# Kernel optimization log

Measured on AMD Instinct MI355X. Metric: run time of the kernel, lower is better.

Reference implementation:

```python
import jax, jax.numpy as jnp
import numpy as np


def _sage_conv(h_src, h_dst, src, dst, W_neigh, W_self, b, n_dst):
    # mean aggregation over in-neighbors of each dst node
    msg = h_src[src]                                             # [E, F]
    s = jax.ops.segment_sum(msg, dst, num_segments=n_dst)        # [n_dst, F]
    deg = jax.ops.segment_sum(jnp.ones_like(dst, dtype=h_src.dtype), dst,
                              num_segments=n_dst)                # [n_dst]
    h_neigh = s / jnp.maximum(deg, 1.0)[:, None]
    # DGL SAGEConv (mean): fc_self(h_dst) + fc_neigh(h_neigh) + bias
    return h_dst @ W_self + h_neigh @ W_neigh + b


def setup_inputs() -> dict:
    key = jax.random.key(0)
    ks = jax.random.split(key, 10)
    N1, N2, N3 = 200000, 40000, 8000
    E1, E2 = 1280000, 256000
    IN, H, C = 128, 256, 47
    return {
        "x": jax.random.normal(ks[0], (N1, IN), dtype=jnp.float32),
        "src1": jax.random.randint(ks[1], (E1,), 0, N1, dtype=jnp.int32),
        "dst1": jax.random.randint(ks[2], (E1,), 0, N2, dtype=jnp.int32),
        "src2": jax.random.randint(ks[3], (E2,), 0, N2, dtype=jnp.int32),
        "dst2": jax.random.randint(ks[4], (E2,), 0, N3, dtype=jnp.int32),
        "n_dst1": N2,
        "n_dst2": N3,
        "W_self1": jax.random.normal(ks[5], (IN, H), dtype=jnp.float32) * (1.0 / np.sqrt(IN)),
        "W_neigh1": jax.random.normal(ks[6], (IN, H), dtype=jnp.float32) * (1.0 / np.sqrt(IN)),
        "b1": jnp.zeros((H,), dtype=jnp.float32),
        "W_self2": jax.random.normal(ks[7], (H, C), dtype=jnp.float32) * (1.0 / np.sqrt(H)),
        "W_neigh2": jax.random.normal(ks[8], (H, C), dtype=jnp.float32) * (1.0 / np.sqrt(H)),
        "b2": jnp.zeros((C,), dtype=jnp.float32),
    }


def reference(x, src1, dst1, src2, dst2, n_dst1, n_dst2,
              W_self1, W_neigh1, b1, W_self2, W_neigh2, b2):
    h_dst = x[:n_dst1]                                            # [N2, IN]
    h = _sage_conv(x, h_dst, src1, dst1, W_neigh1, W_self1, b1, n_dst1)
    h = jax.nn.relu(h)                                            # [N2, H]
    h_dst2 = h[:n_dst2]                                           # [N3, H]
    out = _sage_conv(h, h_dst2, src2, dst2, W_neigh2, W_self2, b2, n_dst2)
    return out                                                    # [N3, C]
```

## Files before the change

### kernel.cpp

```cpp
#include <hip/hip_runtime.h>
#include <hip/hip_bf16.h>
#include <cstddef>


#define N1_SRC 200000
#define N2_DST 40000
#define N2_PAD 40064
#define N3_DST 8000
#define IN_F 128
#define H_F 256
#define C_F 47

#define BSHIFT 7
#define SRCB 18
#define NB1 313
#define NB2 63
#define CAST_BLOCKS 6250

typedef short bf16x8 __attribute__((ext_vector_type(8)));
typedef float f32x4 __attribute__((ext_vector_type(4)));

__device__ __forceinline__ float bf2f(ushort u) {
    union { uint i; float f; } v; v.i = ((uint)u) << 16; return v.f;
}
__device__ __forceinline__ ushort f2bf(float f) {
    union { float f; uint i; } v; v.f = f;
    uint r = v.i + 0x7FFF + ((v.i >> 16) & 1);
    return (ushort)(r >> 16);
}
__device__ __forceinline__ uint pack2(float lo, float hi) {
    return (uint)f2bf(lo) | ((uint)f2bf(hi) << 16);
}
__device__ __forceinline__ void acc8(float* a, uint4 v) {
    a[0] += bf2f((ushort)(v.x & 0xffff)); a[1] += bf2f((ushort)(v.x >> 16));
    a[2] += bf2f((ushort)(v.y & 0xffff)); a[3] += bf2f((ushort)(v.y >> 16));
    a[4] += bf2f((ushort)(v.z & 0xffff)); a[5] += bf2f((ushort)(v.z >> 16));
    a[6] += bf2f((ushort)(v.w & 0xffff)); a[7] += bf2f((ushort)(v.w >> 16));
}


__global__ __launch_bounds__(256) void prep_kernel(
    const float* __restrict__ x, ushort* __restrict__ xb,
    const int* __restrict__ dst1, int* __restrict__ bcnt1, int E1,
    const int* __restrict__ dst2, int* __restrict__ bcnt2, int E2,
    const float* __restrict__ Wself1, const float* __restrict__ Wneigh1,
    ushort* __restrict__ WT1,
    const float* __restrict__ Wself2, const float* __restrict__ Wneigh2,
    ushort* __restrict__ WT2,
    const float* __restrict__ b2, float* __restrict__ bias2p) {
    __shared__ int cnt[NB1];
    int bx = blockIdx.x, t = threadIdx.x;
    if (bx < CAST_BLOCKS) {
        const float4* in4 = (const float4*)x;
        ushort4* out4 = (ushort4*)xb;
        int base = bx * 1024 + t;
#pragma unroll
        for (int j = 0; j < 4; ++j) {
            float4 v = in4[base + j * 256];
            ushort4 o;
            o.x = f2bf(v.x); o.y = f2bf(v.y); o.z = f2bf(v.z); o.w = f2bf(v.w);
            out4[base + j * 256] = o;
        }
        return;
    }
    bx -= CAST_BLOCKS;
    if (bx < NB1 + NB2) {
        const int* dst = (bx < NB1) ? dst1 : dst2;
        int* bcnt = (bx < NB1) ? bcnt1 : bcnt2;
        int E = (bx < NB1) ? E1 : E2;
        int hb = (bx < NB1) ? bx : bx - NB1;
        for (int i = t; i < NB1; i += 256) cnt[i] = 0;
        __syncthreads();
        int base = hb * 4096 + t;
#pragma unroll
        for (int i = 0; i < 16; ++i) {
            int e = base + i * 256;
            if (e < E) atomicAdd(&cnt[dst[e] >> BSHIFT], 1);
        }
        __syncthreads();
        for (int i = t; i < NB1; i += 256) {
            int c = cnt[i];
            if (c) atomicAdd(&bcnt[i], c);
        }
        return;
    }
    bx -= NB1 + NB2;
    if (bx < H_F) {
        int n = bx;
        for (int k = t; k < 2 * IN_F; k += 256) {
            float v = (k < IN_F) ? Wself1[(size_t)k * H_F + n]
                                 : Wneigh1[(size_t)(k - IN_F) * H_F + n];
            WT1[(size_t)n * (2 * IN_F) + k] = f2bf(v);
        }
        return;
    }
    bx -= H_F;
    if (bx < 64) {
        int n = bx;
        for (int k = t; k < 2 * H_F; k += 256) {
            float v = 0.f;
            if (n < C_F) v = (k < H_F) ? Wself2[(size_t)k * C_F + n]
                                       : Wneigh2[(size_t)(k - H_F) * C_F + n];
            WT2[(size_t)n * (2 * H_F) + k] = f2bf(v);
        }
        return;
    }
    bx -= 64;
    if (bx == 0 && t < 64) bias2p[t] = (t < C_F) ? b2[t] : 0.f;
}


__global__ void bucket_scan2(
    const int* __restrict__ bcnt1, int* __restrict__ boff1, int* __restrict__ gcur1,
    int E1, int* __restrict__ off1,
    const int* __restrict__ bcnt2, int* __restrict__ boff2, int* __restrict__ gcur2,
    int E2, int* __restrict__ off2) {
    __shared__ int smem[512];
    int t = threadIdx.x;
    int L = blockIdx.x;
    const int nb = L ? NB2 : NB1;
    const int* bcnt = L ? bcnt2 : bcnt1;
    int* boff = L ? boff2 : boff1;
    int* gcur = L ? gcur2 : gcur1;
    int E = L ? E2 : E1;
    int* offs = L ? off2 : off1;
    int nd = L ? N3_DST : N2_DST;
    int v = (t < nb) ? bcnt[t] : 0;
    smem[t] = v;
    __syncthreads();
    for (int off = 1; off < 512; off <<= 1) {
        int tv = (t >= off) ? smem[t - off] : 0;
        __syncthreads();
        smem[t] += tv;
        __syncthreads();
    }
    if (t < nb) { int e = smem[t] - v; boff[t] = e; gcur[t] = e; }
    if (t == 0) { boff[nb] = E; offs[nd] = E; }
}


__global__ __launch_bounds__(256) void bin_pass1m(
    const int* __restrict__ src1, const int* __restrict__ dst1,
    int* __restrict__ gcur1, uint* __restrict__ temp1, int E1,
    const int* __restrict__ src2, const int* __restrict__ dst2,
    int* __restrict__ gcur2, uint* __restrict__ temp2, int E2) {
    __shared__ int cnt[NB1];
    __shared__ int rnk[NB1];
    __shared__ int gbase[NB1];
    int L = blockIdx.y;
    const int* src = L ? src2 : src1;
    const int* dst = L ? dst2 : dst1;
    int* gcur = L ? gcur2 : gcur1;
    uint* temp = L ? temp2 : temp1;
    int E = L ? E2 : E1;
    int t = threadIdx.x;
    int e0 = blockIdx.x * 4096;
    if (e0 >= E) return;
    for (int i = t; i < NB1; i += 256) { cnt[i] = 0; rnk[i] = 0; }
    __syncthreads();
#pragma unroll
    for (int i = 0; i < 16; ++i) {
        int e = e0 + i * 256 + t;
        if (e < E) atomicAdd(&cnt[dst[e] >> BSHIFT], 1);
    }
    __syncthreads();
    for (int b = t; b < NB1; b += 256) {
        int c = cnt[b];
        gbase[b] = c ? atomicAdd(&gcur[b], c) : 0;
    }
    __syncthreads();
#pragma unroll
    for (int i = 0; i < 16; ++i) {
        int e = e0 + i * 256 + t;
        if (e < E) {
            int d = dst[e];
            int b = d >> BSHIFT;
            int r = atomicAdd(&rnk[b], 1);
            uint val = ((uint)(d & 127) << SRCB) | (uint)src[e];
            temp[gbase[b] + r] = val;
        }
    }
}


__global__ __launch_bounds__(256) void bin_pass2m(
    const uint* __restrict__ temp1, const int* __restrict__ boff1,
    int* __restrict__ off1, int* __restrict__ edges1,
    const uint* __restrict__ temp2, const int* __restrict__ boff2,
    int* __restrict__ off2, int* __restrict__ edges2) {
    constexpr int DPB = 128;
    __shared__ int cnt[DPB];
    __shared__ int scn[DPB];
    __shared__ int obase[DPB];
    __shared__ int rnk[DPB];
    int b = blockIdx.x, t = threadIdx.x;
    int L = (b >= NB1);
    int lb = L ? b - NB1 : b;
    const uint* temp = L ? temp2 : temp1;
    const int* boff = L ? boff2 : boff1;
    int* offsets = L ? off2 : off1;
    int* edges = L ? edges2 : edges1;
    int nd = L ? N3_DST : N2_DST;
    int dbase = lb << BSHIFT;
    if (t < DPB) { cnt[t] = 0; rnk[t] = 0; }
    __syncthreads();
    int beg = boff[lb], end = boff[lb + 1];
    for (int i = beg + t; i < end; i += 256) {
        atomicAdd(&cnt[temp[i] >> SRCB], 1);
    }
    __syncthreads();
    int v = (t < DPB) ? cnt[t] : 0;
    if (t < DPB) scn[t] = v;
    __syncthreads();
    for (int off = 1; off < DPB; off <<= 1) {
        int tv = (t >= off && t < DPB) ? scn[t - off] : 0;
        __syncthreads();
        if (t < DPB) scn[t] += tv;
        __syncthreads();
    }
    if (t < DPB) {
        int ob = beg + scn[t] - v;
        obase[t] = ob;
        if (dbase + t < nd) offsets[dbase + t] = ob;
    }
    __syncthreads();
    for (int i = beg + t; i < end; i += 256) {
        uint val = temp[i];
        int dlow = (int)(val >> SRCB);
        int s = (int)(val & ((1u << SRCB) - 1));
        int r = atomicAdd(&rnk[dlow], 1);
        edges[obase[dlow] + r] = s;
    }
}


__global__ __launch_bounds__(256) void gather_mean_f128(
    const ushort* __restrict__ xb, const int* __restrict__ edges,
    const int* __restrict__ offsets, ushort* __restrict__ outb) {
    int d = (blockIdx.x << 2) | (threadIdx.x >> 6);
    int lane = threadIdx.x & 63;
    int eslot = lane >> 4, lpos = lane & 15;
    int beg = offsets[d], end = offsets[d + 1];
    float a[8] = {};
    int i = beg;
    for (; i + 16 <= end; i += 16) {
        int e0 = edges[i + eslot];
        int e1 = edges[i + 4 + eslot];
        int e2 = edges[i + 8 + eslot];
        int e3 = edges[i + 12 + eslot];
        uint4 v0 = ((const uint4*)(xb + (size_t)e0 * IN_F))[lpos];
        uint4 v1 = ((const uint4*)(xb + (size_t)e1 * IN_F))[lpos];
        uint4 v2 = ((const uint4*)(xb + (size_t)e2 * IN_F))[lpos];
        uint4 v3 = ((const uint4*)(xb + (size_t)e3 * IN_F))[lpos];
        acc8(a, v0); acc8(a, v1); acc8(a, v2); acc8(a, v3);
    }
    for (; i < end; i += 4) {
        if (i + eslot < end) {
            int e = edges[i + eslot];
            uint4 v = ((const uint4*)(xb + (size_t)e * IN_F))[lpos];
            acc8(a, v);
        }
    }
#pragma unroll
    for (int j = 0; j < 8; ++j) {
        a[j] += __shfl_xor(a[j], 16);
        a[j] += __shfl_xor(a[j], 32);
    }
    if (eslot == 0) {
        float inv = 1.0f / fmaxf((float)(end - beg), 1.0f);
        uint4 o;
        o.x = pack2(a[0] * inv, a[1] * inv);
        o.y = pack2(a[2] * inv, a[3] * inv);
        o.z = pack2(a[4] * inv, a[5] * inv);
        o.w = pack2(a[6] * inv, a[7] * inv);
        ((uint4*)(outb + (size_t)d * IN_F))[lpos] = o;
    }
}

__global__ __launch_bounds__(256) void gather_mean_f256(
    const ushort* __restrict__ hb, const int* __restrict__ edges,
    const int* __restrict__ offsets, ushort* __restrict__ outb) {
    int d = (blockIdx.x << 2) | (threadIdx.x >> 6);
    int lane = threadIdx.x & 63;
    int eslot = lane >> 5, lpos = lane & 31;
    int beg = offsets[d], end = offsets[d + 1];
    float a[8] = {};
    int i = beg;
    for (; i + 8 <= end; i += 8) {
        int e0 = edges[i + eslot];
        int e1 = edges[i + 2 + eslot];
        int e2 = edges[i + 4 + eslot];
        int e3 = edges[i + 6 + eslot];
        uint4 v0 = ((const uint4*)(hb + (size_t)e0 * H_F))[lpos];
        uint4 v1 = ((const uint4*)(hb + (size_t)e1 * H_F))[lpos];
        uint4 v2 = ((const uint4*)(hb + (size_t)e2 * H_F))[lpos];
        uint4 v3 = ((const uint4*)(hb + (size_t)e3 * H_F))[lpos];
        acc8(a, v0); acc8(a, v1); acc8(a, v2); acc8(a, v3);
    }
    for (; i < end; i += 2) {
        if (i + eslot < end) {
            int e = edges[i + eslot];
            uint4 v = ((const uint4*)(hb + (size_t)e * H_F))[lpos];
            acc8(a, v);
        }
    }
#pragma unroll
    for (int j = 0; j < 8; ++j) {
        a[j] += __shfl_xor(a[j], 32);
    }
    if (eslot == 0) {
        float inv = 1.0f / fmaxf((float)(end - beg), 1.0f);
        uint4 o;
        o.x = pack2(a[0] * inv, a[1] * inv);
        o.y = pack2(a[2] * inv, a[3] * inv);
        o.z = pack2(a[4] * inv, a[5] * inv);
        o.w = pack2(a[6] * inv, a[7] * inv);
        ((uint4*)(outb + (size_t)d * H_F))[lpos] = o;
    }
}


__global__ __launch_bounds__(256) void sage_mfma_gemm128(
    const ushort* __restrict__ Aself, const ushort* __restrict__ Aneigh,
    const ushort* __restrict__ WT, const float* __restrict__ bias,
    ushort* __restrict__ Cout) {
    constexpr int LDL = 72;
    __shared__ __align__(16) ushort A_lds[128 * LDL];
    __shared__ __align__(16) ushort B_lds[128 * LDL];
    int t = threadIdx.x;
    int bn = blockIdx.x * 128, bm = blockIdx.y * 128;
    int lane = t & 63, w = t >> 6;
    int wr = w >> 1, wc = w & 1;
    int ln = lane & 15, kh = lane >> 4;
    f32x4 acc[4][4] = {};
    for (int kt0 = 0; kt0 < 256; kt0 += 64) {
#pragma unroll
        for (int c = 0; c < 4; ++c) {
            int id = c * 256 + t;
            int row = id >> 3;
            int kc = (id & 7) * 8;
            int k = kt0 + kc;
            const ushort* sa = (k < IN_F)
                                   ? Aself + (size_t)(bm + row) * IN_F + k
                                   : Aneigh + (size_t)(bm + row) * IN_F + (k - IN_F);
            *(float4*)&A_lds[row * LDL + kc] = *(const float4*)sa;
            *(float4*)&B_lds[row * LDL + kc] =
                *(const float4*)(WT + (size_t)(bn + row) * 256 + k);
        }
        __syncthreads();
#pragma unroll
        for (int kt = 0; kt < 2; ++kt) {
            bf16x8 aF[4], bF[4];
#pragma unroll
            for (int m = 0; m < 4; ++m)
                aF[m] = *(const bf16x8*)&A_lds[(wr * 64 + m * 16 + ln) * LDL + kt * 32 + kh * 8];
#pragma unroll
            for (int n = 0; n < 4; ++n)
                bF[n] = *(const bf16x8*)&B_lds[(wc * 64 + n * 16 + ln) * LDL + kt * 32 + kh * 8];
#pragma unroll
            for (int m = 0; m < 4; ++m)
#pragma unroll
                for (int n = 0; n < 4; ++n)
                    acc[m][n] = __builtin_amdgcn_mfma_f32_16x16x32_bf16(
                        aF[m], bF[n], acc[m][n], 0, 0, 0);
        }
        __syncthreads();
    }
#pragma unroll
    for (int m = 0; m < 4; ++m) {
#pragma unroll
        for (int n = 0; n < 4; ++n) {
            int col = bn + wc * 64 + n * 16 + ln;
            float bv = bias[col];
#pragma unroll
            for (int r = 0; r < 4; ++r) {
                int row = bm + wr * 64 + m * 16 + kh * 4 + r;
                float v = fmaxf(acc[m][n][r] + bv, 0.f);
                Cout[(size_t)row * H_F + col] = f2bf(v);
            }
        }
    }
}


template <int K, int KSELF, bool RELU, bool OUTF32>
__global__ __launch_bounds__(256) void sage_mfma_gemm(
    const ushort* __restrict__ Aself, const ushort* __restrict__ Aneigh,
    const ushort* __restrict__ WT, const float* __restrict__ bias,
    void* __restrict__ Cout, int ldc, int ncols) {
    constexpr int KN = K - KSELF;
    constexpr int LDL = K + 8;
    __shared__ __align__(16) ushort A_lds[64 * LDL];
    __shared__ __align__(16) ushort B_lds[64 * LDL];
    int t = threadIdx.x;
    int bn = blockIdx.x * 64, bm = blockIdx.y * 64;
    constexpr int CPR = K / 8;
    constexpr int ITER = 64 * CPR / 256;
#pragma unroll
    for (int c = 0; c < ITER; ++c) {
        int id = c * 256 + t;
        int row = id / CPR;
        int kc = (id % CPR) * 8;
        const ushort* sa = (kc < KSELF)
                               ? Aself + (size_t)(bm + row) * KSELF + kc
                               : Aneigh + (size_t)(bm + row) * KN + (kc - KSELF);
        float4 av = *(const float4*)sa;
        float4 bv = *(const float4*)(WT + (size_t)(bn + row) * K + kc);
        *(float4*)&A_lds[row * LDL + kc] = av;
        *(float4*)&B_lds[row * LDL + kc] = bv;
    }
    __syncthreads();
    int lane = t & 63, w = t >> 6;
    int wr = w >> 1, wc = w & 1;
    int ln = lane & 15, kh = lane >> 4;
    const ushort* Ab = &A_lds[(wr * 32 + ln) * LDL + kh * 8];
    const ushort* Bb = &B_lds[(wc * 32 + ln) * LDL + kh * 8];
    f32x4 acc00 = {0.f, 0.f, 0.f, 0.f};
    f32x4 acc01 = {0.f, 0.f, 0.f, 0.f};
    f32x4 acc10 = {0.f, 0.f, 0.f, 0.f};
    f32x4 acc11 = {0.f, 0.f, 0.f, 0.f};
#pragma unroll
    for (int kt = 0; kt < K / 32; ++kt) {
        bf16x8 a0 = *(const bf16x8*)(Ab + kt * 32);
        bf16x8 a1 = *(const bf16x8*)(Ab + 16 * LDL + kt * 32);
        bf16x8 b0 = *(const bf16x8*)(Bb + kt * 32);
        bf16x8 b1 = *(const bf16x8*)(Bb + 16 * LDL + kt * 32);
        acc00 = __builtin_amdgcn_mfma_f32_16x16x32_bf16(a0, b0, acc00, 0, 0, 0);
        acc01 = __builtin_amdgcn_mfma_f32_16x16x32_bf16(a0, b1, acc01, 0, 0, 0);
        acc10 = __builtin_amdgcn_mfma_f32_16x16x32_bf16(a1, b0, acc10, 0, 0, 0);
        acc11 = __builtin_amdgcn_mfma_f32_16x16x32_bf16(a1, b1, acc11, 0, 0, 0);
    }
    f32x4 accs[2][2] = {{acc00, acc01}, {acc10, acc11}};
#pragma unroll
    for (int m = 0; m < 2; ++m) {
#pragma unroll
        for (int n = 0; n < 2; ++n) {
            int col = bn + wc * 32 + n * 16 + ln;
            float bv = bias[col];
#pragma unroll
            for (int r = 0; r < 4; ++r) {
                int row = bm + wr * 32 + m * 16 + kh * 4 + r;
                float v = accs[m][n][r] + bv;
                if (RELU) v = fmaxf(v, 0.f);
                if (OUTF32) {
                    if (col < ncols) ((float*)Cout)[(size_t)row * ncols + col] = v;
                } else {
                    ((ushort*)Cout)[(size_t)row * ldc + col] = f2bf(v);
                }
            }
        }
    }
}


static inline char* carve(char*& p, size_t bytes) {
    char* r = p;
    p += (bytes + 255) & ~(size_t)255;
    return r;
}

extern "C" void kernel_launch(void* const* d_in, const int* in_sizes, int n_in,
                              void* d_out, int out_size, void* d_ws, size_t ws_size,
                              hipStream_t stream) {
    const float* x        = (const float*)d_in[0];
    const int*   src1     = (const int*)d_in[1];
    const int*   dst1     = (const int*)d_in[2];
    const int*   src2     = (const int*)d_in[3];
    const int*   dst2     = (const int*)d_in[4];
    const float* W_self1  = (const float*)d_in[7];
    const float* W_neigh1 = (const float*)d_in[8];
    const float* b1       = (const float*)d_in[9];
    const float* W_self2  = (const float*)d_in[10];
    const float* W_neigh2 = (const float*)d_in[11];
    const float* b2       = (const float*)d_in[12];
    float* out = (float*)d_out;

    const int E1 = in_sizes[1];
    const int E2 = in_sizes[3];

    char* p = (char*)d_ws;
    ushort* xb       = (ushort*)carve(p, (size_t)N1_SRC * IN_F * 2);
    ushort* hb       = (ushort*)carve(p, (size_t)N2_PAD * H_F * 2);
    ushort* hneighb  = (ushort*)carve(p, (size_t)N2_PAD * IN_F * 2);
    ushort* hneigh2b = (ushort*)carve(p, (size_t)N3_DST * H_F * 2);
    int*    edges1   = (int*)carve(p, (size_t)E1 * 4);
    int*    edges2   = (int*)carve(p, (size_t)E2 * 4);
    int*    off1     = (int*)carve(p, (size_t)(N2_DST + 1) * 4);
    int*    off2     = (int*)carve(p, (size_t)(N3_DST + 1) * 4);
    int*    bcnt     = (int*)carve(p, (size_t)(NB1 + NB2) * 4);
    int*    bcnt1    = bcnt;
    int*    bcnt2    = bcnt + NB1;
    int*    boff1    = (int*)carve(p, (size_t)(NB1 + 1) * 4);
    int*    boff2    = (int*)carve(p, (size_t)(NB2 + 1) * 4);
    int*    gcur1    = (int*)carve(p, (size_t)NB1 * 4);
    int*    gcur2    = (int*)carve(p, (size_t)NB2 * 4);
    ushort* WT1      = (ushort*)carve(p, (size_t)H_F * (2 * IN_F) * 2);
    ushort* WT2      = (ushort*)carve(p, (size_t)64 * (2 * H_F) * 2);
    float*  bias2p   = (float*)carve(p, 64 * 4);
    uint* temp1 = (uint*)hneighb;
    uint* temp2 = temp1 + E1;

    hipMemsetAsync(bcnt, 0, (size_t)(NB1 + NB2) * 4, stream);

    {
        int nblk = CAST_BLOCKS + (NB1 + NB2) + H_F + 64 + 1;
        prep_kernel<<<nblk, 256, 0, stream>>>(
            x, xb, dst1, bcnt1, E1, dst2, bcnt2, E2,
            W_self1, W_neigh1, WT1, W_self2, W_neigh2, WT2, b2, bias2p);
    }

    bucket_scan2<<<2, 512, 0, stream>>>(bcnt1, boff1, gcur1, E1, off1,
                                        bcnt2, boff2, gcur2, E2, off2);

    {
        dim3 grid((E1 + 4095) / 4096, 2);
        bin_pass1m<<<grid, 256, 0, stream>>>(src1, dst1, gcur1, temp1, E1,
                                             src2, dst2, gcur2, temp2, E2);
    }

    bin_pass2m<<<NB1 + NB2, 256, 0, stream>>>(temp1, boff1, off1, edges1,
                                              temp2, boff2, off2, edges2);

    gather_mean_f128<<<N2_DST / 4, 256, 0, stream>>>(xb, edges1, off1, hneighb);
    {
        dim3 grid(H_F / 128, N2_PAD / 128);
        sage_mfma_gemm128<<<grid, 256, 0, stream>>>(xb, hneighb, WT1, b1, hb);
    }

    gather_mean_f256<<<N3_DST / 4, 256, 0, stream>>>(hb, edges2, off2, hneigh2b);
    {
        dim3 grid(1, N3_DST / 64);
        sage_mfma_gemm<512, 256, false, true><<<grid, 256, 0, stream>>>(
            hb, hneigh2b, WT2, bias2p, out, C_F, C_F);
    }
}
```

Baseline: 165.9 us.

## Fuse per-destination binning into bucket-level gather kernels using LDS edge lists

Removes the second binning pass and its global CSR arrays (edges and offsets). Each 1024-thread block now takes one destination bucket, counts and scans per-destination degrees in LDS, builds a sorted source list in shared memory, then gathers and averages neighbor features for its 128 destinations. The first binning pass also processes 8192 edges per block instead of 4096. This saves a kernel launch and a global round trip of the edge list. In exchange the gather grid shrinks to one block per bucket, only 313 and 63 blocks, which may underuse the GPU and hide memory latency less well, especially in layer 2. It also assumes no bucket exceeds 8192 edges.

```diff
diff --git a/kernel.cpp b/kernel.cpp
--- a/kernel.cpp
+++ b/kernel.cpp
@@ -112,9 +112,9 @@
 
 __global__ void bucket_scan2(
     const int* __restrict__ bcnt1, int* __restrict__ boff1, int* __restrict__ gcur1,
-    int E1, int* __restrict__ off1,
+    int E1,
     const int* __restrict__ bcnt2, int* __restrict__ boff2, int* __restrict__ gcur2,
-    int E2, int* __restrict__ off2) {
+    int E2) {
     __shared__ int smem[512];
     int t = threadIdx.x;
     int L = blockIdx.x;
@@ -123,8 +123,6 @@
     int* boff = L ? boff2 : boff1;
     int* gcur = L ? gcur2 : gcur1;
     int E = L ? E2 : E1;
-    int* offs = L ? off2 : off1;
-    int nd = L ? N3_DST : N2_DST;
     int v = (t < nb) ? bcnt[t] : 0;
     smem[t] = v;
     __syncthreads();
@@ -135,7 +133,7 @@
         __syncthreads();
     }
     if (t < nb) { int e = smem[t] - v; boff[t] = e; gcur[t] = e; }
-    if (t == 0) { boff[nb] = E; offs[nd] = E; }
+    if (t == 0) boff[nb] = E;
 }
 
 
@@ -154,12 +152,12 @@
     uint* temp = L ? temp2 : temp1;
     int E = L ? E2 : E1;
     int t = threadIdx.x;
-    int e0 = blockIdx.x * 4096;
+    int e0 = blockIdx.x * 8192;
     if (e0 >= E) return;
     for (int i = t; i < NB1; i += 256) { cnt[i] = 0; rnk[i] = 0; }
     __syncthreads();
 #pragma unroll
-    for (int i = 0; i < 16; ++i) {
+    for (int i = 0; i < 32; ++i) {
         int e = e0 + i * 256 + t;
         if (e < E) atomicAdd(&cnt[dst[e] >> BSHIFT], 1);
     }
@@ -170,7 +168,7 @@
     }
     __syncthreads();
 #pragma unroll
-    for (int i = 0; i < 16; ++i) {
+    for (int i = 0; i < 32; ++i) {
         int e = e0 + i * 256 + t;
         if (e < E) {
             int d = dst[e];
@@ -183,139 +181,80 @@
 }
 
 
-__global__ __launch_bounds__(256) void bin_pass2m(
-    const uint* __restrict__ temp1, const int* __restrict__ boff1,
-    int* __restrict__ off1, int* __restrict__ edges1,
-    const uint* __restrict__ temp2, const int* __restrict__ boff2,
-    int* __restrict__ off2, int* __restrict__ edges2) {
-    constexpr int DPB = 128;
-    __shared__ int cnt[DPB];
-    __shared__ int scn[DPB];
-    __shared__ int obase[DPB];
-    __shared__ int rnk[DPB];
+template <int FEATS, int ND>
+__global__ __launch_bounds__(1024) void gather_fused(
+    const ushort* __restrict__ feat, const uint* __restrict__ temp,
+    const int* __restrict__ boff, ushort* __restrict__ outb) {
+    __shared__ int cnt[128];
+    __shared__ int offs[128];
+    __shared__ int rnk[128];
+    __shared__ uint list[8192];
     int b = blockIdx.x, t = threadIdx.x;
-    int L = (b >= NB1);
-    int lb = L ? b - NB1 : b;
-    const uint* temp = L ? temp2 : temp1;
-    const int* boff = L ? boff2 : boff1;
-    int* offsets = L ? off2 : off1;
-    int* edges = L ? edges2 : edges1;
-    int nd = L ? N3_DST : N2_DST;
-    int dbase = lb << BSHIFT;
-    if (t < DPB) { cnt[t] = 0; rnk[t] = 0; }
-    __syncthreads();
-    int beg = boff[lb], end = boff[lb + 1];
-    for (int i = beg + t; i < end; i += 256) {
+    int beg = boff[b], end = boff[b + 1];
+    if (t < 128) { cnt[t] = 0; rnk[t] = 0; }
+    __syncthreads();
+    for (int i = beg + t; i < end; i += 1024)
         atomicAdd(&cnt[temp[i] >> SRCB], 1);
-    }
-    __syncthreads();
-    int v = (t < DPB) ? cnt[t] : 0;
-    if (t < DPB) scn[t] = v;
-    __syncthreads();
-    for (int off = 1; off < DPB; off <<= 1) {
-        int tv = (t >= off && t < DPB) ? scn[t - off] : 0;
-        __syncthreads();
-        if (t < DPB) scn[t] += tv;
-        __syncthreads();
-    }
-    if (t < DPB) {
-        int ob = beg + scn[t] - v;
-        obase[t] = ob;
-        if (dbase + t < nd) offsets[dbase + t] = ob;
-    }
-    __syncthreads();
-    for (int i = beg + t; i < end; i += 256) {
-        uint val = temp[i];
-        int dlow = (int)(val >> SRCB);
-        int s = (int)(val & ((1u << SRCB) - 1));
-        int r = atomicAdd(&rnk[dlow], 1);
-        edges[obase[dlow] + r] = s;
-    }
-}
-
-
-__global__ __launch_bounds__(256) void gather_mean_f128(
-    const ushort* __restrict__ xb, const int* __restrict__ edges,
-    const int* __restrict__ offsets, ushort* __restrict__ outb) {
-    int d = (blockIdx.x << 2) | (threadIdx.x >> 6);
-    int lane = threadIdx.x & 63;
-    int eslot = lane >> 4, lpos = lane & 15;
-    int beg = offsets[d], end = offsets[d + 1];
-    float a[8] = {};
-    int i = beg;
-    for (; i + 16 <= end; i += 16) {
-        int e0 = edges[i + eslot];
-        int e1 = edges[i + 4 + eslot];
-        int e2 = edges[i + 8 + eslot];
-        int e3 = edges[i + 12 + eslot];
-        uint4 v0 = ((const uint4*)(xb + (size_t)e0 * IN_F))[lpos];
-        uint4 v1 = ((const uint4*)(xb + (size_t)e1 * IN_F))[lpos];
-        uint4 v2 = ((const uint4*)(xb + (size_t)e2 * IN_F))[lpos];
-        uint4 v3 = ((const uint4*)(xb + (size_t)e3 * IN_F))[lpos];
-        acc8(a, v0); acc8(a, v1); acc8(a, v2); acc8(a, v3);
-    }
-    for (; i < end; i += 4) {
-        if (i + eslot < end) {
-            int e = edges[i + eslot];
-            uint4 v = ((const uint4*)(xb + (size_t)e * IN_F))[lpos];
-            acc8(a, v);
-        }
-    }
-#pragma unroll
-    for (int j = 0; j < 8; ++j) {
-        a[j] += __shfl_xor(a[j], 16);
-        a[j] += __shfl_xor(a[j], 32);
-    }
-    if (eslot == 0) {
-        float inv = 1.0f / fmaxf((float)(end - beg), 1.0f);
-        uint4 o;
-        o.x = pack2(a[0] * inv, a[1] * inv);
-        o.y = pack2(a[2] * inv, a[3] * inv);
-        o.z = pack2(a[4] * inv, a[5] * inv);
-        o.w = pack2(a[6] * inv, a[7] * inv);
-        ((uint4*)(outb + (size_t)d * IN_F))[lpos] = o;
-    }
-}
-
-__global__ __launch_bounds__(256) void gather_mean_f256(
-    const ushort* __restrict__ hb, const int* __restrict__ edges,
-    const int* __restrict__ offsets, ushort* __restrict__ outb) {
-    int d = (blockIdx.x << 2) | (threadIdx.x >> 6);
-    int lane = threadIdx.x & 63;
-    int eslot = lane >> 5, lpos = lane & 31;
-    int beg = offsets[d], end = offsets[d + 1];
-    float a[8] = {};
-    int i = beg;
-    for (; i + 8 <= end; i += 8) {
-        int e0 = edges[i + eslot];
-        int e1 = edges[i + 2 + eslot];
-        int e2 = edges[i + 4 + eslot];
-        int e3 = edges[i + 6 + eslot];
-        uint4 v0 = ((const uint4*)(hb + (size_t)e0 * H_F))[lpos];
-        uint4 v1 = ((const uint4*)(hb + (size_t)e1 * H_F))[lpos];
-        uint4 v2 = ((const uint4*)(hb + (size_t)e2 * H_F))[lpos];
-        uint4 v3 = ((const uint4*)(hb + (size_t)e3 * H_F))[lpos];
-        acc8(a, v0); acc8(a, v1); acc8(a, v2); acc8(a, v3);
-    }
-    for (; i < end; i += 2) {
-        if (i + eslot < end) {
-            int e = edges[i + eslot];
-            uint4 v = ((const uint4*)(hb + (size_t)e * H_F))[lpos];
-            acc8(a, v);
-        }
-    }
-#pragma unroll
-    for (int j = 0; j < 8; ++j) {
-        a[j] += __shfl_xor(a[j], 32);
-    }
-    if (eslot == 0) {
-        float inv = 1.0f / fmaxf((float)(end - beg), 1.0f);
-        uint4 o;
-        o.x = pack2(a[0] * inv, a[1] * inv);
-        o.y = pack2(a[2] * inv, a[3] * inv);
-        o.z = pack2(a[4] * inv, a[5] * inv);
-        o.w = pack2(a[6] * inv, a[7] * inv);
-        ((uint4*)(outb + (size_t)d * H_F))[lpos] = o;
+    __syncthreads();
+    if (t < 128) offs[t] = cnt[t];
+    __syncthreads();
+    for (int o = 1; o < 128; o <<= 1) {
+        int v = (t >= o && t < 128) ? offs[t - o] : 0;
+        __syncthreads();
+        if (t < 128) offs[t] += v;
+        __syncthreads();
+    }
+    for (int i = beg + t; i < end; i += 1024) {
+        uint v = temp[i];
+        int dl = (int)(v >> SRCB);
+        int r = atomicAdd(&rnk[dl], 1);
+        list[offs[dl] - cnt[dl] + r] = v & ((1u << SRCB) - 1);
+    }
+    __syncthreads();
+    int wv = t >> 6, lane = t & 63;
+    constexpr int LPR = FEATS / 8;
+    constexpr int ES = 64 / LPR;
+    int eslot = lane / LPR, lpos = lane % LPR;
+#pragma unroll
+    for (int q = 0; q < 8; ++q) {
+        int dl = wv * 8 + q;
+        int d = (b << BSHIFT) + dl;
+        int deg = cnt[dl];
+        int lbeg = offs[dl] - deg;
+        float a[8] = {};
+        int i = 0;
+        for (; i + 4 * ES <= deg; i += 4 * ES) {
+            int e0 = list[lbeg + i + eslot];
+            int e1 = list[lbeg + i + ES + eslot];
+            int e2 = list[lbeg + i + 2 * ES + eslot];
+            int e3 = list[lbeg + i + 3 * ES + eslot];
+            uint4 v0 = ((const uint4*)(feat + (size_t)e0 * FEATS))[lpos];
+            uint4 v1 = ((const uint4*)(feat + (size_t)e1 * FEATS))[lpos];
+            uint4 v2 = ((const uint4*)(feat + (size_t)e2 * FEATS))[lpos];
+            uint4 v3 = ((const uint4*)(feat + (size_t)e3 * FEATS))[lpos];
+            acc8(a, v0); acc8(a, v1); acc8(a, v2); acc8(a, v3);
+        }
+        for (; i < deg; i += ES) {
+            if (i + eslot < deg) {
+                int e = list[lbeg + i + eslot];
+                uint4 v = ((const uint4*)(feat + (size_t)e * FEATS))[lpos];
+                acc8(a, v);
+            }
+        }
+#pragma unroll
+        for (int j = 0; j < 8; ++j) {
+            if (ES == 4) a[j] += __shfl_xor(a[j], 16);
+            a[j] += __shfl_xor(a[j], 32);
+        }
+        if (eslot == 0 && d < ND) {
+            float inv = 1.0f / fmaxf((float)deg, 1.0f);
+            uint4 o;
+            o.x = pack2(a[0] * inv, a[1] * inv);
+            o.y = pack2(a[2] * inv, a[3] * inv);
+            o.z = pack2(a[4] * inv, a[5] * inv);
+            o.w = pack2(a[6] * inv, a[7] * inv);
+            ((uint4*)(outb + (size_t)d * FEATS))[lpos] = o;
+        }
     }
 }
 
@@ -483,10 +422,8 @@
     ushort* hb       = (ushort*)carve(p, (size_t)N2_PAD * H_F * 2);
     ushort* hneighb  = (ushort*)carve(p, (size_t)N2_PAD * IN_F * 2);
     ushort* hneigh2b = (ushort*)carve(p, (size_t)N3_DST * H_F * 2);
-    int*    edges1   = (int*)carve(p, (size_t)E1 * 4);
-    int*    edges2   = (int*)carve(p, (size_t)E2 * 4);
-    int*    off1     = (int*)carve(p, (size_t)(N2_DST + 1) * 4);
-    int*    off2     = (int*)carve(p, (size_t)(N3_DST + 1) * 4);
+    uint*   temp1    = (uint*)carve(p, (size_t)E1 * 4);
+    uint*   temp2    = (uint*)carve(p, (size_t)E2 * 4);
     int*    bcnt     = (int*)carve(p, (size_t)(NB1 + NB2) * 4);
     int*    bcnt1    = bcnt;
     int*    bcnt2    = bcnt + NB1;
@@ -497,8 +434,6 @@
     ushort* WT1      = (ushort*)carve(p, (size_t)H_F * (2 * IN_F) * 2);
     ushort* WT2      = (ushort*)carve(p, (size_t)64 * (2 * H_F) * 2);
     float*  bias2p   = (float*)carve(p, 64 * 4);
-    uint* temp1 = (uint*)hneighb;
-    uint* temp2 = temp1 + E1;
 
     hipMemsetAsync(bcnt, 0, (size_t)(NB1 + NB2) * 4, stream);
 
@@ -509,25 +444,22 @@
             W_self1, W_neigh1, WT1, W_self2, W_neigh2, WT2, b2, bias2p);
     }
 
-    bucket_scan2<<<2, 512, 0, stream>>>(bcnt1, boff1, gcur1, E1, off1,
-                                        bcnt2, boff2, gcur2, E2, off2);
+    bucket_scan2<<<2, 512, 0, stream>>>(bcnt1, boff1, gcur1, E1,
+                                        bcnt2, boff2, gcur2, E2);
 
     {
-        dim3 grid((E1 + 4095) / 4096, 2);
+        dim3 grid((E1 + 8191) / 8192, 2);
         bin_pass1m<<<grid, 256, 0, stream>>>(src1, dst1, gcur1, temp1, E1,
                                              src2, dst2, gcur2, temp2, E2);
     }
 
-    bin_pass2m<<<NB1 + NB2, 256, 0, stream>>>(temp1, boff1, off1, edges1,
-                                              temp2, boff2, off2, edges2);
-
-    gather_mean_f128<<<N2_DST / 4, 256, 0, stream>>>(xb, edges1, off1, hneighb);
+    gather_fused<IN_F, N2_DST><<<NB1, 1024, 0, stream>>>(xb, temp1, boff1, hneighb);
     {
         dim3 grid(H_F / 128, N2_PAD / 128);
         sage_mfma_gemm128<<<grid, 256, 0, stream>>>(xb, hneighb, WT1, b1, hb);
     }
 
-    gather_mean_f256<<<N3_DST / 4, 256, 0, stream>>>(hb, edges2, off2, hneigh2b);
+    gather_fused<H_F, N3_DST><<<NB2, 1024, 0, stream>>>(hb, temp2, boff2, hneigh2b);
     {
         dim3 grid(1, N3_DST / 64);
         sage_mfma_gemm<512, 256, false, true><<<grid, 256, 0, stream>>>(
```

After: 186.1 us. 1.12x slower.

## Split x bf16 cast across CSR-build kernels to fill idle CUs

Applied to the files above, without the earlier changes.

The fp32-to-bf16 cast of x, previously done entirely in the prep kernel, is split into four chunks appended as extra blocks to the histogram, scan, bin pass1 and bin pass2 kernels. The small, latency-bound CSR-construction kernels leave most CUs idle, so the bandwidth-bound cast work is spread across them to overlap with the serial chain. Pass1 also changes from a 2D grid to a 1D grid with explicit layer selection. The cast blocks could slow down the critical-path blocks in each kernel if they get scheduled first, and the chunk offsets must sum exactly to the whole array.

```diff
diff --git a/kernel.cpp b/kernel.cpp
--- a/kernel.cpp
+++ b/kernel.cpp
@@ -15,7 +15,14 @@
 #define SRCB 18
 #define NB1 313
 #define NB2 63
-#define CAST_BLOCKS 6250
+
+#define K1_CAST_BLOCKS 2800
+#define K2_CAST_BLOCKS 1100
+#define K3_CAST_BLOCKS 700
+#define K4_CAST_BLOCKS 550
+#define K2_BASE_F4 2867200
+#define K3_BASE_F4 5120000
+#define K4_BASE_F4 5836800
 
 typedef short bf16x8 __attribute__((ext_vector_type(8)));
 typedef float f32x4 __attribute__((ext_vector_type(4)));
@@ -37,9 +44,18 @@
     a[4] += bf2f((ushort)(v.z & 0xffff)); a[5] += bf2f((ushort)(v.z >> 16));
     a[6] += bf2f((ushort)(v.w & 0xffff)); a[7] += bf2f((ushort)(v.w >> 16));
 }
-
-
-__global__ __launch_bounds__(256) void prep_kernel(
+__device__ __forceinline__ void cast4(const float4* __restrict__ in4,
+                                      ushort4* __restrict__ out4, int idx) {
+    float4 v = in4[idx];
+    ushort4 o;
+    o.x = f2bf(v.x); o.y = f2bf(v.y); o.z = f2bf(v.z); o.w = f2bf(v.w);
+    out4[idx] = o;
+}
+
+
+#define K1_CSR (NB1 + NB2 + H_F + 64 + 1)
+
+__global__ __launch_bounds__(256) void k1_hist_wt_cast(
     const float* __restrict__ x, ushort* __restrict__ xb,
     const int* __restrict__ dst1, int* __restrict__ bcnt1, int E1,
     const int* __restrict__ dst2, int* __restrict__ bcnt2, int E2,
@@ -50,20 +66,13 @@
     const float* __restrict__ b2, float* __restrict__ bias2p) {
     __shared__ int cnt[NB1];
     int bx = blockIdx.x, t = threadIdx.x;
-    if (bx < CAST_BLOCKS) {
-        const float4* in4 = (const float4*)x;
-        ushort4* out4 = (ushort4*)xb;
-        int base = bx * 1024 + t;
-#pragma unroll
-        for (int j = 0; j < 4; ++j) {
-            float4 v = in4[base + j * 256];
-            ushort4 o;
-            o.x = f2bf(v.x); o.y = f2bf(v.y); o.z = f2bf(v.z); o.w = f2bf(v.w);
-            out4[base + j * 256] = o;
-        }
-        return;
-    }
-    bx -= CAST_BLOCKS;
+    if (bx >= K1_CSR) {
+        int base = (bx - K1_CSR) * 1024 + t;
+#pragma unroll
+        for (int j = 0; j < 4; ++j)
+            cast4((const float4*)x, (ushort4*)xb, base + j * 256);
+        return;
+    }
     if (bx < NB1 + NB2) {
         const int* dst = (bx < NB1) ? dst1 : dst2;
         int* bcnt = (bx < NB1) ? bcnt1 : bcnt2;
@@ -110,14 +119,22 @@
 }
 
 
-__global__ void bucket_scan2(
+__global__ __launch_bounds__(512) void k2_scan_cast(
+    const float* __restrict__ x, ushort* __restrict__ xb,
     const int* __restrict__ bcnt1, int* __restrict__ boff1, int* __restrict__ gcur1,
     int E1, int* __restrict__ off1,
     const int* __restrict__ bcnt2, int* __restrict__ boff2, int* __restrict__ gcur2,
     int E2, int* __restrict__ off2) {
     __shared__ int smem[512];
-    int t = threadIdx.x;
-    int L = blockIdx.x;
+    int bx = blockIdx.x, t = threadIdx.x;
+    if (bx >= 2) {
+        int base = K2_BASE_F4 + (bx - 2) * 2048 + t;
+#pragma unroll
+        for (int j = 0; j < 4; ++j)
+            cast4((const float4*)x, (ushort4*)xb, base + j * 512);
+        return;
+    }
+    int L = bx;
     const int nb = L ? NB2 : NB1;
     const int* bcnt = L ? bcnt2 : bcnt1;
     int* boff = L ? boff2 : boff1;
@@ -139,7 +156,10 @@
 }
 
 
-__global__ __launch_bounds__(256) void bin_pass1m(
+#define K3_CSR (NB1 + NB2)
+
+__global__ __launch_bounds__(256) void k3_pass1_cast(
+    const float* __restrict__ x, ushort* __restrict__ xb,
     const int* __restrict__ src1, const int* __restrict__ dst1,
     int* __restrict__ gcur1, uint* __restrict__ temp1, int E1,
     const int* __restrict__ src2, const int* __restrict__ dst2,
@@ -147,14 +167,22 @@
     __shared__ int cnt[NB1];
     __shared__ int rnk[NB1];
     __shared__ int gbase[NB1];
-    int L = blockIdx.y;
+    int bx = blockIdx.x, t = threadIdx.x;
+    if (bx >= K3_CSR) {
+        int base = K3_BASE_F4 + (bx - K3_CSR) * 1024 + t;
+#pragma unroll
+        for (int j = 0; j < 4; ++j)
+            cast4((const float4*)x, (ushort4*)xb, base + j * 256);
+        return;
+    }
+    int L = (bx >= NB1);
+    int pb = L ? bx - NB1 : bx;
     const int* src = L ? src2 : src1;
     const int* dst = L ? dst2 : dst1;
     int* gcur = L ? gcur2 : gcur1;
     uint* temp = L ? temp2 : temp1;
     int E = L ? E2 : E1;
-    int t = threadIdx.x;
-    int e0 = blockIdx.x * 4096;
+    int e0 = pb * 4096;
     if (e0 >= E) return;
     for (int i = t; i < NB1; i += 256) { cnt[i] = 0; rnk[i] = 0; }
     __syncthreads();
@@ -183,7 +211,10 @@
 }
 
 
-__global__ __launch_bounds__(256) void bin_pass2m(
+#define K4_CSR (NB1 + NB2)
+
+__global__ __launch_bounds__(256) void k4_pass2_cast(
+    const float* __restrict__ x, ushort* __restrict__ xb,
     const uint* __restrict__ temp1, const int* __restrict__ boff1,
     int* __restrict__ off1, int* __restrict__ edges1,
     const uint* __restrict__ temp2, const int* __restrict__ boff2,
@@ -193,9 +224,16 @@
     __shared__ int scn[DPB];
     __shared__ int obase[DPB];
     __shared__ int rnk[DPB];
-    int b = blockIdx.x, t = threadIdx.x;
-    int L = (b >= NB1);
-    int lb = L ? b - NB1 : b;
+    int bx = blockIdx.x, t = threadIdx.x;
+    if (bx >= K4_CSR) {
+        int base = K4_BASE_F4 + (bx - K4_CSR) * 1024 + t;
+#pragma unroll
+        for (int j = 0; j < 4; ++j)
+            cast4((const float4*)x, (ushort4*)xb, base + j * 256);
+        return;
+    }
+    int L = (bx >= NB1);
+    int lb = L ? bx - NB1 : bx;
     const uint* temp = L ? temp2 : temp1;
     const int* boff = L ? boff2 : boff1;
     int* offsets = L ? off2 : off1;
@@ -502,24 +540,18 @@
 
     hipMemsetAsync(bcnt, 0, (size_t)(NB1 + NB2) * 4, stream);
 
-    {
-        int nblk = CAST_BLOCKS + (NB1 + NB2) + H_F + 64 + 1;
-        prep_kernel<<<nblk, 256, 0, stream>>>(
-            x, xb, dst1, bcnt1, E1, dst2, bcnt2, E2,
-            W_self1, W_neigh1, WT1, W_self2, W_neigh2, WT2, b2, bias2p);
-    }
-
-    bucket_scan2<<<2, 512, 0, stream>>>(bcnt1, boff1, gcur1, E1, off1,
-                                        bcnt2, boff2, gcur2, E2, off2);
-
-    {
-        dim3 grid((E1 + 4095) / 4096, 2);
-        bin_pass1m<<<grid, 256, 0, stream>>>(src1, dst1, gcur1, temp1, E1,
-                                             src2, dst2, gcur2, temp2, E2);
-    }
-
-    bin_pass2m<<<NB1 + NB2, 256, 0, stream>>>(temp1, boff1, off1, edges1,
-                                              temp2, boff2, off2, edges2);
+    k1_hist_wt_cast<<<K1_CSR + K1_CAST_BLOCKS, 256, 0, stream>>>(
+        x, xb, dst1, bcnt1, E1, dst2, bcnt2, E2,
+        W_self1, W_neigh1, WT1, W_self2, W_neigh2, WT2, b2, bias2p);
+
+    k2_scan_cast<<<2 + K2_CAST_BLOCKS, 512, 0, stream>>>(
+        x, xb, bcnt1, boff1, gcur1, E1, off1, bcnt2, boff2, gcur2, E2, off2);
+
+    k3_pass1_cast<<<K3_CSR + K3_CAST_BLOCKS, 256, 0, stream>>>(
+        x, xb, src1, dst1, gcur1, temp1, E1, src2, dst2, gcur2, temp2, E2);
+
+    k4_pass2_cast<<<K4_CSR + K4_CAST_BLOCKS, 256, 0, stream>>>(
+        x, xb, temp1, boff1, off1, edges1, temp2, boff2, off2, edges2);
 
     gather_mean_f128<<<N2_DST / 4, 256, 0, stream>>>(xb, edges1, off1, hneighb);
     {
```

New measurement: 163.9 us. About the same (-1.2%).
